# Performance work log

Hardware: AMD Instinct MI355X
Metric: run time of the kernel (lower is better)

## Reference

```python
import jax, jax.numpy as jnp
import numpy as np

K = 3
K2 = K * K
EPS = 1e-5


def conv2d(x, w, stride=1, pad=1):
    return jax.lax.conv_general_dilated(
        x, w, (stride, stride), [(pad, pad), (pad, pad)],
        dimension_numbers=("NCHW", "OIHW", "NCHW"))


def bilinear_sample(x, py, px):
    """x: [B,C,H,W]; py,px: [B,Ho,Wo,K2] float sample coords.
    Zero padding outside bounds (torchvision deform_conv2d semantics).
    Returns [B,C,Ho,Wo,K2]."""
    B, C, H, W = x.shape
    Ho, Wo = py.shape[1], py.shape[2]
    y0 = jnp.floor(py)
    x0 = jnp.floor(px)
    wy1 = py - y0
    wx1 = px - x0
    x_flat = x.reshape(B, C, H * W)

    def gather(yi, xi):
        valid = (yi >= 0) & (yi < H) & (xi >= 0) & (xi < W)
        yc = jnp.clip(yi, 0, H - 1).astype(jnp.int32)
        xc = jnp.clip(xi, 0, W - 1).astype(jnp.int32)
        idx = (yc * W + xc).reshape(B, 1, -1)          # [B,1,N]
        v = jnp.take_along_axis(x_flat, idx, axis=2)   # [B,C,N]
        return v * valid.reshape(B, 1, -1).astype(x.dtype)

    w00 = ((1 - wy1) * (1 - wx1)).reshape(B, 1, -1)
    w01 = ((1 - wy1) * wx1).reshape(B, 1, -1)
    w10 = (wy1 * (1 - wx1)).reshape(B, 1, -1)
    w11 = (wy1 * wx1).reshape(B, 1, -1)
    val = (w00 * gather(y0, x0) + w01 * gather(y0, x0 + 1)
           + w10 * gather(y0 + 1, x0) + w11 * gather(y0 + 1, x0 + 1))
    return val.reshape(B, C, Ho, Wo, K2)


def deform_conv_bn_relu(x, d, offset_w, conv_w, gamma, beta):
    # offset branch: 3x3 conv on d, clamp to [-1,1]
    offset = jnp.clip(conv2d(d, offset_w, 1, 1), -1.0, 1.0)  # [B,2*K2,H,W]
    B, Cin, H, W = x.shape
    Cout = conv_w.shape[0]
    off = offset.reshape(B, K2, 2, H, W)
    dy = off[:, :, 0].transpose(0, 2, 3, 1)  # [B,H,W,K2]
    dx = off[:, :, 1].transpose(0, 2, 3, 1)
    kh = (jnp.arange(K2) // K).astype(jnp.float32)
    kw = (jnp.arange(K2) % K).astype(jnp.float32)
    # sample coords: out pixel + kernel tap - padding + learned offset
    py = (jnp.arange(H, dtype=jnp.float32)[None, :, None, None] - 1.0
          + kh[None, None, None, :] + dy)
    px = (jnp.arange(W, dtype=jnp.float32)[None, None, :, None] - 1.0
          + kw[None, None, None, :] + dx)
    sampled = bilinear_sample(x, py, px)  # [B,Cin,H,W,K2]
    out = jnp.einsum('bchwk,ock->bohw', sampled,
                     conv_w.reshape(Cout, Cin, K2))
    # BatchNorm2d (training forward: biased batch stats) + ReLU
    mean = out.mean(axis=(0, 2, 3))
    var = out.var(axis=(0, 2, 3))
    inv = gamma / jnp.sqrt(var + EPS)
    out = (out - mean[None, :, None, None]) * inv[None, :, None, None] \
        + beta[None, :, None, None]
    out = jax.nn.relu(out)
    return out, offset


def setup_inputs() -> dict:
    key = jax.random.key(0)
    k1, k2, k3, k4 = jax.random.split(key, 4)
    B, C, H, W = 4, 64, 160, 160
    Cout, offC = 64, 64
    x = jax.random.normal(k1, (B, C, H, W), dtype=jnp.float32)
    d = jax.random.normal(k2, (B, offC, H, W), dtype=jnp.float32)
    # torch zero-inits offset_conv; use small random weights so the
    # bilinear gather path is actually exercised with fractional offsets
    offset_w = jax.random.normal(k3, (2 * K2, offC, K, K), dtype=jnp.float32) * 0.01
    conv_w = jax.random.normal(k4, (Cout, C, K, K), dtype=jnp.float32) * (1.0 / np.sqrt(C * K2))
    gamma = jnp.ones((Cout,), dtype=jnp.float32)
    beta = jnp.zeros((Cout,), dtype=jnp.float32)
    return {"x": x, "d": d, "offset_w": offset_w, "conv_w": conv_w,
            "gamma": gamma, "beta": beta}


def reference(x, d, offset_w, conv_w, gamma, beta):
    return deform_conv_bn_relu(x, d, offset_w, conv_w, gamma, beta)
```

## Files before the change

kernel.cpp:

```cpp
#include <hip/hip_runtime.h>
#include <hip/hip_fp16.h>

#define BB 4
#define HH 160
#define WW 160
#define HWD (HH * WW)
#define OUT_ELEMS (BB * 64 * HWD)
#define EPSBN 1e-5f
#define CHSTRIDE (8 * HWD)
#define NSLOT 256

typedef _Float16 f16x8 __attribute__((ext_vector_type(8)));
typedef __attribute__((ext_vector_type(4))) float f32x4;

__device__ inline unsigned short f16bits(float a) {
  _Float16 h = (_Float16)a;
  unsigned short u;
  __builtin_memcpy(&u, &h, 2);
  return u;
}
__device__ inline unsigned packh2(float a, float b) {
  return (unsigned)f16bits(a) | ((unsigned)f16bits(b) << 16);
}

__device__ inline void tile_map(int blk, int& b, int& ty0, int& tx0) {
  int t = (blk & 7) * 200 + (blk >> 3);
  b = t / 400;
  int r = t % 400;
  ty0 = (r / 10) * 4;
  tx0 = (r % 10) * 16;
}

__global__ void prep_kernel(const float* __restrict__ cw,
                            const float* __restrict__ ow,
                            unsigned short* __restrict__ Bp,
                            unsigned short* __restrict__ B2p,
                            float* __restrict__ part) {
  int i = blockIdx.x * 256 + threadIdx.x;
  if (i < 32768) part[i] = 0.f;
  if (i < 49152) {
    int j = i & 7, l = (i >> 3) & 63, rest = i >> 9;
    int ki = rest % 24, nt = rest / 24;
    int kp = ki * 32 + ((l >> 4) << 3) + j;
    int chunk = kp / 96, kq = kp % 96;
    int t = kq >> 3, c = kq & 7;
    int n = nt * 16 + (l & 15);
    float v = (t < 9) ? cw[n * 576 + (chunk * 8 + c) * 9 + t] : 0.f;
    Bp[i] = f16bits(v);
  }
  if (i < 24576) {
    int j = i & 7, l = (i >> 3) & 63, rest = i >> 9;
    int ki = rest % 24, nt = rest / 24;
    int kp = ki * 32 + ((l >> 4) << 3) + j;
    int chunk = kp / 96, kq = kp % 96;
    int t = kq >> 3, c = kq & 7;
    int n = nt * 16 + (l & 15);
    float v = (t < 9 && n < 18) ? ow[n * 576 + (chunk * 8 + c) * 9 + t] : 0.f;
    B2p[i] = f16bits(v);
  }
}

__global__ __launch_bounds__(256) void fused_kernel(
    const float* __restrict__ x, const float* __restrict__ d,
    const f16x8* __restrict__ Bp, const f16x8* __restrict__ B2p,
    float* __restrict__ out, float* __restrict__ off_out,
    float* __restrict__ part) {
  int b, ty0, tx0;
  tile_map(blockIdx.x, b, ty0, tx0);
  const int tid = threadIdx.x;
  const int wv = tid >> 6, lane = tid & 63;
  const int lo = lane >> 4, li = lane & 15;

  __shared__ __align__(16) unsigned patch2[756];
  __shared__ f16x8 Af[768];
  __shared__ __align__(16) float offbuf[64 * 19];

  int gdo[2];
  bool gdk[2];
#pragma unroll
  for (int i = 0; i < 2; ++i) {
    int l = tid + i * 256;
    int p = l >> 2, c2 = l & 3;
    int r = p / 18, col = p % 18;
    int gy = ty0 - 1 + r, gx = tx0 - 1 + col;
    gdk[i] = (l < 432) && gy >= 0 && gy < HH && gx >= 0 && gx < WW;
    gdo[i] = ((b * 64 + 2 * c2) * HH + gy) * WW + gx;
  }
  unsigned gd[2];
#pragma unroll
  for (int i = 0; i < 2; ++i)
    gd[i] = gdk[i] ? packh2(d[gdo[i]], d[gdo[i] + HWD]) : 0u;

  int gxo[3];
  bool gxk[3];
#pragma unroll
  for (int i = 0; i < 3; ++i) {
    int l = tid + i * 256;
    int p = l >> 2, c2 = l & 3;
    int r = p / 21, col = p % 21;
    int gy = ty0 - 2 + r, gx2 = tx0 - 2 + col;
    gxk[i] = (l < 756) && gy >= 0 && gy < HH && gx2 >= 0 && gx2 < WW;
    gxo[i] = ((b * 64 + 2 * c2) * HH + gy) * WW + gx2;
  }
  unsigned gx[3];

  f32x4 acc0{0.f, 0.f, 0.f, 0.f}, acc1{0.f, 0.f, 0.f, 0.f};
  const int nt = wv >> 1, mh = wv & 1;
  int poffA[3];
#pragma unroll
  for (int kk = 0; kk < 3; ++kk) {
    int t = kk * 4 + lo;
    if (t > 8) t = 8;
    poffA[kk] = ((t / 3) * 18 + t % 3 + li) * 4;
  }

  for (int chunk = 0; chunk < 8; ++chunk) {
    f16x8 bw0 = B2p[((nt * 24 + chunk * 3 + 0) << 6) + lane];
    f16x8 bw1 = B2p[((nt * 24 + chunk * 3 + 1) << 6) + lane];
    f16x8 bw2 = B2p[((nt * 24 + chunk * 3 + 2) << 6) + lane];
#pragma unroll
    for (int i = 0; i < 2; ++i) {
      int l = tid + i * 256;
      if (l < 432) patch2[l] = gd[i];
    }
    __syncthreads();
    if (chunk < 7) {
      int nco = (chunk + 1) * CHSTRIDE;
#pragma unroll
      for (int i = 0; i < 2; ++i)
        gd[i] = gdk[i] ? packh2(d[gdo[i] + nco], d[gdo[i] + nco + HWD]) : 0u;
    } else {
#pragma unroll
      for (int i = 0; i < 3; ++i)
        gx[i] = gxk[i] ? packh2(x[gxo[i]], x[gxo[i] + HWD]) : 0u;
    }
#pragma unroll
    for (int kk = 0; kk < 3; ++kk) {
      f16x8 bw = (kk == 0) ? bw0 : (kk == 1) ? bw1 : bw2;
      const f16x8* a0 = (const f16x8*)(patch2 + poffA[kk] + (mh * 2) * 72);
      const f16x8* a1 = (const f16x8*)(patch2 + poffA[kk] + (mh * 2 + 1) * 72);
      acc0 = __builtin_amdgcn_mfma_f32_16x16x32_f16(*a0, bw, acc0, 0, 0, 0);
      acc1 = __builtin_amdgcn_mfma_f32_16x16x32_f16(*a1, bw, acc1, 0, 0, 0);
    }
    __syncthreads();
  }

  const int nA = nt * 16 + li;
  if (nA < 18) {
#pragma unroll
    for (int f = 0; f < 2; ++f) {
      int mf = mh * 2 + f;
      f32x4 a = f ? acc1 : acc0;
      float4 v;
      v.x = fminf(1.f, fmaxf(-1.f, a[0]));
      v.y = fminf(1.f, fmaxf(-1.f, a[1]));
      v.z = fminf(1.f, fmaxf(-1.f, a[2]));
      v.w = fminf(1.f, fmaxf(-1.f, a[3]));
      offbuf[(mf * 16 + lo * 4 + 0) * 19 + nA] = v.x;
      offbuf[(mf * 16 + lo * 4 + 1) * 19 + nA] = v.y;
      offbuf[(mf * 16 + lo * 4 + 2) * 19 + nA] = v.z;
      offbuf[(mf * 16 + lo * 4 + 3) * 19 + nA] = v.w;
      *(float4*)(off_out + ((b * 18 + nA) * HH + ty0 + mf) * WW + tx0 +
                 lo * 4) = v;
    }
  }
  __syncthreads();

  const int h = ty0 + wv, w = tx0 + li;
  const int m_pix = wv * 16 + li;
  int bs[3];
  bool tre[3];
  __half2 w00h[3], w01h[3], w10h[3], w11h[3];
#pragma unroll
  for (int kk = 0; kk < 3; ++kk) {
    int t = kk * 4 + lo;
    tre[kk] = (t < 9);
    if (tre[kk]) {
      float dy = offbuf[m_pix * 19 + 2 * t];
      float dx = offbuf[m_pix * 19 + 2 * t + 1];
      float pyf = (float)(h - 1 + t / 3) + dy;
      float pxf = (float)(w - 1 + t % 3) + dx;
      float y0 = floorf(pyf), x0 = floorf(pxf);
      float wy = pyf - y0, wx = pxf - x0;
      bs[kk] = (((int)y0 - (ty0 - 2)) * 21 + ((int)x0 - (tx0 - 2))) * 4;
      w00h[kk] = __float2half2_rn((1.f - wy) * (1.f - wx));
      w01h[kk] = __float2half2_rn((1.f - wy) * wx);
      w10h[kk] = __float2half2_rn(wy * (1.f - wx));
      w11h[kk] = __float2half2_rn(wy * wx);
    } else {
      bs[kk] = 0;
      w00h[kk] = w01h[kk] = w10h[kk] = w11h[kk] = __float2half2_rn(0.f);
    }
  }

  f32x4 acc[4];
#pragma unroll
  for (int i = 0; i < 4; ++i) acc[i] = f32x4{0.f, 0.f, 0.f, 0.f};

  union u4h { uint4 q; __half2 hh[4]; unsigned u[4]; f16x8 v; };

  for (int chunk = 0; chunk < 8; ++chunk) {
    f16x8 bw0 = Bp[((wv * 24 + chunk * 3 + 0) << 6) + lane];
    f16x8 bw1 = Bp[((wv * 24 + chunk * 3 + 1) << 6) + lane];
    f16x8 bw2 = Bp[((wv * 24 + chunk * 3 + 2) << 6) + lane];
#pragma unroll
    for (int i = 0; i < 3; ++i) {
      int l = tid + i * 256;
      if (l < 756) patch2[l] = gx[i];
    }
    __syncthreads();
    if (chunk < 7) {
      int nco = (chunk + 1) * CHSTRIDE;
#pragma unroll
      for (int i = 0; i < 3; ++i)
        gx[i] = gxk[i] ? packh2(x[gxo[i] + nco], x[gxo[i] + nco + HWD]) : 0u;
    }
#pragma unroll
    for (int kk = 0; kk < 3; ++kk) {
      u4h a;
      if (tre[kk]) {
        u4h q00, q01, q10, q11;
        q00.q = *(const uint4*)(patch2 + bs[kk]);
        q01.q = *(const uint4*)(patch2 + bs[kk] + 4);
        q10.q = *(const uint4*)(patch2 + bs[kk] + 84);
        q11.q = *(const uint4*)(patch2 + bs[kk] + 88);
#pragma unroll
        for (int j = 0; j < 4; ++j) {
          __half2 v = __hmul2(w00h[kk], q00.hh[j]);
          v = __hfma2(w01h[kk], q01.hh[j], v);
          v = __hfma2(w10h[kk], q10.hh[j], v);
          v = __hfma2(w11h[kk], q11.hh[j], v);
          a.hh[j] = v;
        }
      } else {
        a.u[0] = a.u[1] = a.u[2] = a.u[3] = 0u;
      }
      Af[((wv * 3 + kk) << 6) + lane] = a.v;
    }
    __syncthreads();
#pragma unroll
    for (int kk = 0; kk < 3; ++kk) {
      f16x8 bw = (kk == 0) ? bw0 : (kk == 1) ? bw1 : bw2;
#pragma unroll
      for (int mf = 0; mf < 4; ++mf)
        acc[mf] = __builtin_amdgcn_mfma_f32_16x16x32_f16(
            Af[((mf * 3 + kk) << 6) + lane], bw, acc[mf], 0, 0, 0);
    }
  }

  const int n = wv * 16 + li;
  float s = 0.f, s2 = 0.f;
#pragma unroll
  for (int mf = 0; mf < 4; ++mf) {
    float* po = out + ((b * 64 + n) * HH + ty0 + mf) * WW + tx0 + lo * 4;
    *(float4*)po = make_float4(acc[mf][0], acc[mf][1], acc[mf][2], acc[mf][3]);
#pragma unroll
    for (int r = 0; r < 4; ++r) {
      float v = acc[mf][r];
      s += v;
      s2 = fmaf(v, v, s2);
    }
  }
  s += __shfl_xor(s, 16);
  s += __shfl_xor(s, 32);
  s2 += __shfl_xor(s2, 16);
  s2 += __shfl_xor(s2, 32);
  if (lo == 0) {
    int slot = blockIdx.x & (NSLOT - 1);
    atomicAdd(&part[n * NSLOT + slot], s);
    atomicAdd(&part[(64 + n) * NSLOT + slot], s2);
  }
}

__global__ __launch_bounds__(256) void bn_final_kernel(
    float* __restrict__ out, const float* __restrict__ part,
    const float* __restrict__ gamma, const float* __restrict__ beta) {
  const int i = blockIdx.x * 256 + threadIdx.x;
  const int o = (i / (HWD / 4)) & 63;
  const int tid = threadIdx.x, wv = tid >> 6;

  float s = part[o * NSLOT + tid];
  float s2 = part[(64 + o) * NSLOT + tid];
#pragma unroll
  for (int sh = 1; sh < 64; sh <<= 1) {
    s += __shfl_xor(s, sh);
    s2 += __shfl_xor(s2, sh);
  }
  __shared__ float red[8];
  if ((tid & 63) == 0) { red[wv] = s; red[4 + wv] = s2; }
  __syncthreads();
  s = red[0] + red[1] + red[2] + red[3];
  s2 = red[4] + red[5] + red[6] + red[7];

  const float n_inv = 1.0f / (float)(BB * HWD);
  float mean = s * n_inv;
  float var = s2 * n_inv - mean * mean;
  float inv = gamma[o] * rsqrtf(var + EPSBN);
  float bt = beta[o];
  float4 v = ((float4*)out)[i];
  v.x = fmaxf(0.f, (v.x - mean) * inv + bt);
  v.y = fmaxf(0.f, (v.y - mean) * inv + bt);
  v.z = fmaxf(0.f, (v.z - mean) * inv + bt);
  v.w = fmaxf(0.f, (v.w - mean) * inv + bt);
  ((float4*)out)[i] = v;
}

extern "C" void kernel_launch(void* const* d_in, const int* in_sizes, int n_in,
                              void* d_out, int out_size, void* d_ws, size_t ws_size,
                              hipStream_t stream) {
  const float* x = (const float*)d_in[0];
  const float* d = (const float*)d_in[1];
  const float* ow = (const float*)d_in[2];
  const float* cw = (const float*)d_in[3];
  const float* gamma = (const float*)d_in[4];
  const float* beta = (const float*)d_in[5];

  float* out = (float*)d_out;
  float* off_out = out + OUT_ELEMS;

  unsigned short* Bp = (unsigned short*)d_ws;
  unsigned short* B2p = Bp + 49152;
  float* part = (float*)(B2p + 24576);

  prep_kernel<<<192, 256, 0, stream>>>(cw, ow, Bp, B2p, part);

  fused_kernel<<<1600, 256, 0, stream>>>(
      x, d, (const f16x8*)Bp, (const f16x8*)B2p, out, off_out, part);

  bn_final_kernel<<<OUT_ELEMS / 4 / 256, 256, 0, stream>>>(
      out, part, gamma, beta);
}
```

Baseline: 173.9 us.

## Double-buffer input patches and feed bilinear samples directly into MFMA per wave

The single shared patch buffer is replaced with two ping-pong buffers for the offset-conv input and the sampled-x input, with a prefetch depth of two chunks. This removes one barrier per chunk and lets global loads overlap with compute. The main GEMM is also remapped so each wave owns one output row and all 64 output channels. Sampled activations go straight from registers into MFMA, which drops the Af shared-memory round trip and its extra barrier. In exchange each wave loads all weight fragments (12 per chunk), which raises register pressure and global/L2 weight traffic.

```diff
diff --git a/kernel.cpp b/kernel.cpp
--- a/kernel.cpp
+++ b/kernel.cpp
@@ -71,8 +71,8 @@
   const int wv = tid >> 6, lane = tid & 63;
   const int lo = lane >> 4, li = lane & 15;
 
-  __shared__ __align__(16) unsigned patch2[756];
-  __shared__ f16x8 Af[768];
+  __shared__ __align__(16) unsigned pA[2][432];
+  __shared__ __align__(16) unsigned pB[2][768];
   __shared__ __align__(16) float offbuf[64 * 19];
 
   int gdo[2];
@@ -82,15 +82,10 @@
     int l = tid + i * 256;
     int p = l >> 2, c2 = l & 3;
     int r = p / 18, col = p % 18;
-    int gy = ty0 - 1 + r, gx = tx0 - 1 + col;
-    gdk[i] = (l < 432) && gy >= 0 && gy < HH && gx >= 0 && gx < WW;
-    gdo[i] = ((b * 64 + 2 * c2) * HH + gy) * WW + gx;
-  }
-  unsigned gd[2];
-#pragma unroll
-  for (int i = 0; i < 2; ++i)
-    gd[i] = gdk[i] ? packh2(d[gdo[i]], d[gdo[i] + HWD]) : 0u;
-
+    int gy = ty0 - 1 + r, gcx = tx0 - 1 + col;
+    gdk[i] = (l < 432) && gy >= 0 && gy < HH && gcx >= 0 && gcx < WW;
+    gdo[i] = ((b * 64 + 2 * c2) * HH + gy) * WW + gcx;
+  }
   int gxo[3];
   bool gxk[3];
 #pragma unroll
@@ -102,65 +97,80 @@
     gxk[i] = (l < 756) && gy >= 0 && gy < HH && gx2 >= 0 && gx2 < WW;
     gxo[i] = ((b * 64 + 2 * c2) * HH + gy) * WW + gx2;
   }
-  unsigned gx[3];
-
-  f32x4 acc0{0.f, 0.f, 0.f, 0.f}, acc1{0.f, 0.f, 0.f, 0.f};
-  const int nt = wv >> 1, mh = wv & 1;
+  unsigned gd[2], gx[3];
+
   int poffA[3];
 #pragma unroll
   for (int kk = 0; kk < 3; ++kk) {
     int t = kk * 4 + lo;
     if (t > 8) t = 8;
-    poffA[kk] = ((t / 3) * 18 + t % 3 + li) * 4;
-  }
-
+    poffA[kk] = ((wv + t / 3) * 18 + li + t % 3) * 4;
+  }
+
+#pragma unroll
+  for (int i = 0; i < 2; ++i)
+    gd[i] = gdk[i] ? packh2(d[gdo[i]], d[gdo[i] + HWD]) : 0u;
+#pragma unroll
+  for (int i = 0; i < 2; ++i) {
+    int l = tid + i * 256;
+    if (l < 432) pA[0][l] = gd[i];
+  }
+#pragma unroll
+  for (int i = 0; i < 2; ++i)
+    gd[i] = gdk[i] ? packh2(d[gdo[i] + CHSTRIDE], d[gdo[i] + CHSTRIDE + HWD])
+                   : 0u;
+  __syncthreads();
+
+  f32x4 accA0{0.f, 0.f, 0.f, 0.f}, accA1{0.f, 0.f, 0.f, 0.f};
   for (int chunk = 0; chunk < 8; ++chunk) {
-    f16x8 bw0 = B2p[((nt * 24 + chunk * 3 + 0) << 6) + lane];
-    f16x8 bw1 = B2p[((nt * 24 + chunk * 3 + 1) << 6) + lane];
-    f16x8 bw2 = B2p[((nt * 24 + chunk * 3 + 2) << 6) + lane];
-#pragma unroll
-    for (int i = 0; i < 2; ++i) {
-      int l = tid + i * 256;
-      if (l < 432) patch2[l] = gd[i];
-    }
-    __syncthreads();
+    const int p = chunk & 1;
+    f16x8 bwA[6];
+#pragma unroll
+    for (int nt = 0; nt < 2; ++nt)
+#pragma unroll
+      for (int kk = 0; kk < 3; ++kk)
+        bwA[nt * 3 + kk] = B2p[((nt * 24 + chunk * 3 + kk) << 6) + lane];
     if (chunk < 7) {
-      int nco = (chunk + 1) * CHSTRIDE;
+#pragma unroll
+      for (int i = 0; i < 2; ++i) {
+        int l = tid + i * 256;
+        if (l < 432) pA[p ^ 1][l] = gd[i];
+      }
+    }
+    if (chunk < 6) {
+      int nco = (chunk + 2) * CHSTRIDE;
 #pragma unroll
       for (int i = 0; i < 2; ++i)
         gd[i] = gdk[i] ? packh2(d[gdo[i] + nco], d[gdo[i] + nco + HWD]) : 0u;
-    } else {
+    } else if (chunk == 6) {
 #pragma unroll
       for (int i = 0; i < 3; ++i)
         gx[i] = gxk[i] ? packh2(x[gxo[i]], x[gxo[i] + HWD]) : 0u;
     }
 #pragma unroll
     for (int kk = 0; kk < 3; ++kk) {
-      f16x8 bw = (kk == 0) ? bw0 : (kk == 1) ? bw1 : bw2;
-      const f16x8* a0 = (const f16x8*)(patch2 + poffA[kk] + (mh * 2) * 72);
-      const f16x8* a1 = (const f16x8*)(patch2 + poffA[kk] + (mh * 2 + 1) * 72);
-      acc0 = __builtin_amdgcn_mfma_f32_16x16x32_f16(*a0, bw, acc0, 0, 0, 0);
-      acc1 = __builtin_amdgcn_mfma_f32_16x16x32_f16(*a1, bw, acc1, 0, 0, 0);
+      f16x8 a = *(const f16x8*)(&pA[p][poffA[kk]]);
+      accA0 = __builtin_amdgcn_mfma_f32_16x16x32_f16(a, bwA[kk], accA0, 0, 0, 0);
+      accA1 = __builtin_amdgcn_mfma_f32_16x16x32_f16(a, bwA[3 + kk], accA1, 0, 0, 0);
     }
     __syncthreads();
   }
 
-  const int nA = nt * 16 + li;
-  if (nA < 18) {
-#pragma unroll
-    for (int f = 0; f < 2; ++f) {
-      int mf = mh * 2 + f;
-      f32x4 a = f ? acc1 : acc0;
+#pragma unroll
+  for (int nt = 0; nt < 2; ++nt) {
+    int n = nt * 16 + li;
+    if (n < 18) {
+      f32x4 a = nt ? accA1 : accA0;
       float4 v;
       v.x = fminf(1.f, fmaxf(-1.f, a[0]));
       v.y = fminf(1.f, fmaxf(-1.f, a[1]));
       v.z = fminf(1.f, fmaxf(-1.f, a[2]));
       v.w = fminf(1.f, fmaxf(-1.f, a[3]));
-      offbuf[(mf * 16 + lo * 4 + 0) * 19 + nA] = v.x;
-      offbuf[(mf * 16 + lo * 4 + 1) * 19 + nA] = v.y;
-      offbuf[(mf * 16 + lo * 4 + 2) * 19 + nA] = v.z;
-      offbuf[(mf * 16 + lo * 4 + 3) * 19 + nA] = v.w;
-      *(float4*)(off_out + ((b * 18 + nA) * HH + ty0 + mf) * WW + tx0 +
+      offbuf[(wv * 16 + lo * 4 + 0) * 19 + n] = v.x;
+      offbuf[(wv * 16 + lo * 4 + 1) * 19 + n] = v.y;
+      offbuf[(wv * 16 + lo * 4 + 2) * 19 + n] = v.z;
+      offbuf[(wv * 16 + lo * 4 + 3) * 19 + n] = v.w;
+      *(float4*)(off_out + ((b * 18 + n) * HH + ty0 + wv) * WW + tx0 +
                  lo * 4) = v;
     }
   }
@@ -193,6 +203,17 @@
     }
   }
 
+#pragma unroll
+  for (int i = 0; i < 3; ++i) {
+    int l = tid + i * 256;
+    if (l < 756) pB[0][l] = gx[i];
+  }
+#pragma unroll
+  for (int i = 0; i < 3; ++i)
+    gx[i] = gxk[i] ? packh2(x[gxo[i] + CHSTRIDE], x[gxo[i] + CHSTRIDE + HWD])
+                   : 0u;
+  __syncthreads();
+
   f32x4 acc[4];
 #pragma unroll
   for (int i = 0; i < 4; ++i) acc[i] = f32x4{0.f, 0.f, 0.f, 0.f};
@@ -200,17 +221,22 @@
   union u4h { uint4 q; __half2 hh[4]; unsigned u[4]; f16x8 v; };
 
   for (int chunk = 0; chunk < 8; ++chunk) {
-    f16x8 bw0 = Bp[((wv * 24 + chunk * 3 + 0) << 6) + lane];
-    f16x8 bw1 = Bp[((wv * 24 + chunk * 3 + 1) << 6) + lane];
-    f16x8 bw2 = Bp[((wv * 24 + chunk * 3 + 2) << 6) + lane];
-#pragma unroll
-    for (int i = 0; i < 3; ++i) {
-      int l = tid + i * 256;
-      if (l < 756) patch2[l] = gx[i];
-    }
-    __syncthreads();
+    const int p = chunk & 1;
+    f16x8 bw[12];
+#pragma unroll
+    for (int nt = 0; nt < 4; ++nt)
+#pragma unroll
+      for (int kk = 0; kk < 3; ++kk)
+        bw[nt * 3 + kk] = Bp[((nt * 24 + chunk * 3 + kk) << 6) + lane];
     if (chunk < 7) {
-      int nco = (chunk + 1) * CHSTRIDE;
+#pragma unroll
+      for (int i = 0; i < 3; ++i) {
+        int l = tid + i * 256;
+        if (l < 756) pB[p ^ 1][l] = gx[i];
+      }
+    }
+    if (chunk < 6) {
+      int nco = (chunk + 2) * CHSTRIDE;
 #pragma unroll
       for (int i = 0; i < 3; ++i)
         gx[i] = gxk[i] ? packh2(x[gxo[i] + nco], x[gxo[i] + nco + HWD]) : 0u;
@@ -220,10 +246,10 @@
       u4h a;
       if (tre[kk]) {
         u4h q00, q01, q10, q11;
-        q00.q = *(const uint4*)(patch2 + bs[kk]);
-        q01.q = *(const uint4*)(patch2 + bs[kk] + 4);
-        q10.q = *(const uint4*)(patch2 + bs[kk] + 84);
-        q11.q = *(const uint4*)(patch2 + bs[kk] + 88);
+        q00.q = *(const uint4*)(&pB[p][bs[kk]]);
+        q01.q = *(const uint4*)(&pB[p][bs[kk] + 4]);
+        q10.q = *(const uint4*)(&pB[p][bs[kk] + 84]);
+        q11.q = *(const uint4*)(&pB[p][bs[kk] + 88]);
 #pragma unroll
         for (int j = 0; j < 4; ++j) {
           __half2 v = __hmul2(w00h[kk], q00.hh[j]);
@@ -235,40 +261,35 @@
       } else {
         a.u[0] = a.u[1] = a.u[2] = a.u[3] = 0u;
       }
-      Af[((wv * 3 + kk) << 6) + lane] = a.v;
+#pragma unroll
+      for (int nt = 0; nt < 4; ++nt)
+        acc[nt] = __builtin_amdgcn_mfma_f32_16x16x32_f16(
+            a.v, bw[nt * 3 + kk], acc[nt], 0, 0, 0);
     }
     __syncthreads();
-#pragma unroll
-    for (int kk = 0; kk < 3; ++kk) {
-      f16x8 bw = (kk == 0) ? bw0 : (kk == 1) ? bw1 : bw2;
-#pragma unroll
-      for (int mf = 0; mf < 4; ++mf)
-        acc[mf] = __builtin_amdgcn_mfma_f32_16x16x32_f16(
-            Af[((mf * 3 + kk) << 6) + lane], bw, acc[mf], 0, 0, 0);
-    }
-  }
-
-  const int n = wv * 16 + li;
-  float s = 0.f, s2 = 0.f;
-#pragma unroll
-  for (int mf = 0; mf < 4; ++mf) {
-    float* po = out + ((b * 64 + n) * HH + ty0 + mf) * WW + tx0 + lo * 4;
-    *(float4*)po = make_float4(acc[mf][0], acc[mf][1], acc[mf][2], acc[mf][3]);
+  }
+
+  int slot = blockIdx.x & (NSLOT - 1);
+#pragma unroll
+  for (int nt = 0; nt < 4; ++nt) {
+    int n = nt * 16 + li;
+    float* po = out + ((b * 64 + n) * HH + ty0 + wv) * WW + tx0 + lo * 4;
+    *(float4*)po = make_float4(acc[nt][0], acc[nt][1], acc[nt][2], acc[nt][3]);
+    float s = 0.f, s2 = 0.f;
 #pragma unroll
     for (int r = 0; r < 4; ++r) {
-      float v = acc[mf][r];
+      float v = acc[nt][r];
       s += v;
       s2 = fmaf(v, v, s2);
     }
-  }
-  s += __shfl_xor(s, 16);
-  s += __shfl_xor(s, 32);
-  s2 += __shfl_xor(s2, 16);
-  s2 += __shfl_xor(s2, 32);
-  if (lo == 0) {
-    int slot = blockIdx.x & (NSLOT - 1);
-    atomicAdd(&part[n * NSLOT + slot], s);
-    atomicAdd(&part[(64 + n) * NSLOT + slot], s2);
+    s += __shfl_xor(s, 16);
+    s += __shfl_xor(s, 32);
+    s2 += __shfl_xor(s2, 16);
+    s2 += __shfl_xor(s2, 32);
+    if (lo == 0) {
+      atomicAdd(&part[n * NSLOT + slot], s);
+      atomicAdd(&part[(64 + n) * NSLOT + slot], s2);
+    }
   }
 }
 
```

After: 226.1 us. +30.0%, slower.
